# Kernel tuning notes

Measured on AMD Instinct MI355X. Metric: run time of the kernel, lower is better.

The kernel has to match this reference:

```python
import jax, jax.numpy as jnp
import numpy as np

B, N, QD = 2, 1024, 512          # batch (ref+feat), tokens (32x32), query_dim
H, DH = 8, 64                    # heads, dim_head
INNER = H * DH
HW = 64                          # raw mask spatial size
SCALE = DH ** (-0.5)


def setup_inputs() -> dict:
    key = jax.random.key(0)
    ks = jax.random.split(key, 6)
    s = 0.02
    x = jax.random.normal(ks[0], (B, N, QD), jnp.float32)
    mask = jax.random.randint(ks[1], (B // 2, 1, HW, HW), 0, 2).astype(jnp.float32)
    Wq = jax.random.normal(ks[2], (INNER, QD), jnp.float32) * s
    Wk = jax.random.normal(ks[3], (INNER, QD), jnp.float32) * s
    Wv = jax.random.normal(ks[4], (INNER, QD), jnp.float32) * s
    # zero_module only zeroes to_out at init; use random weights for a meaningful baseline
    Wo = jax.random.normal(ks[5], (QD, INNER), jnp.float32) * s
    bo = jnp.zeros((QD,), jnp.float32)
    return {"x": x, "mask": mask, "Wq": Wq, "Wk": Wk, "Wv": Wv, "Wo": Wo, "bo": bo, "share": 1}


def nearest_resize(m, size):
    # PyTorch F.interpolate(mode='nearest'): src = floor(dst * in/out)
    ih = (jnp.arange(size) * m.shape[-2]) // size
    iw = (jnp.arange(size) * m.shape[-1]) // size
    return m[:, :, ih][:, :, :, iw]


def adain(feat, ref, mask):
    # feat, ref: (b, n, d); mask: (b, n, 1) binary
    ref_std = jnp.std(ref, axis=-2, keepdims=True, ddof=1)   # torch std is unbiased
    ref_mean = jnp.mean(ref, axis=-2, keepdims=True)
    cnt = jnp.sum(mask, axis=-2, keepdims=True)              # (b,1,1)
    f_mean = jnp.sum(feat * mask, axis=-2, keepdims=True) / cnt
    f_var = jnp.sum(mask * (feat - f_mean) ** 2, axis=-2, keepdims=True) / (cnt - 1.0)
    f_std = jnp.sqrt(f_var)
    new = (feat - f_mean) / f_std * ref_std + ref_mean
    return new * mask + feat * (1.0 - mask)


def split_heads(t):
    b, n, _ = t.shape
    return t.reshape(b, n, H, DH).transpose(0, 2, 1, 3).reshape(b * H, n, DH)


def reference(x, mask, Wq, Wk, Wv, Wo, bo, share):
    q = x @ Wq.T
    k = x @ Wk.T
    v = x @ Wv.T
    size = int(N ** 0.5)  # 32
    m = nearest_resize(mask, size).reshape(-1, N, 1)  # (B//2, N, 1)
    ref_k, feat_k = k[: B // 2], k[B // 2:]
    ref_v, feat_v = v[: B // 2], v[B // 2:]
    feat_k = adain(feat_k, ref_k, m)
    feat_v = adain(feat_v, ref_v, m)
    k = jnp.concatenate([ref_k, feat_k], axis=0)
    v = jnp.concatenate([ref_v, feat_v], axis=0)
    k = jnp.concatenate([k, jnp.tile(ref_k, (2, 1, 1))], axis=1)  # (B, 2N, INNER)
    v = jnp.concatenate([v, jnp.tile(ref_v, (2, 1, 1))], axis=1)
    qh, kh, vh = split_heads(q), split_heads(k), split_heads(v)
    sim = jnp.einsum('bid,bjd->bij', qh, kh) * SCALE  # (B*H, N, 2N)
    am = jnp.tile(m, (H, 1, N))                       # (B//2*H, N, N)
    am = (1.0 - am) * (-1e9)
    am = jnp.concatenate([jnp.zeros_like(am), am], axis=0)   # (B*H, N, N)
    am = jnp.concatenate([jnp.zeros_like(am), am], axis=-1)  # (B*H, N, 2N)
    attn = jax.nn.softmax(sim + am, axis=-1)
    out = jnp.einsum('bij,bjd->bid', attn, vh)               # (B*H, N, DH)
    out = out.reshape(B, H, N, DH).transpose(0, 2, 1, 3).reshape(B, N, INNER)
    return out @ Wo.T + bo
```

## Files before the change

### kernel.cpp

```cpp
#include <hip/hip_runtime.h>
#include <math.h>

#define NTOK 1024
#define QDIM 512
#define NH 8
#define DHD 64

using s16x8 = __attribute__((ext_vector_type(8))) short;
using f32x4 = __attribute__((ext_vector_type(4))) float;

__device__ __forceinline__ unsigned short f2bf(float x) {
  union { float f; unsigned u; } v; v.f = x;
  unsigned r = (v.u + 0x7fffu + ((v.u >> 16) & 1u)) >> 16;
  return (unsigned short)r;
}
__device__ __forceinline__ float bf2f(unsigned short h) {
  union { unsigned u; float f; } v; v.u = ((unsigned)h) << 16;
  return v.f;
}
__device__ __forceinline__ unsigned cvt_pk_bf16(float lo, float hi) {
  unsigned r;
  asm volatile("v_cvt_pk_bf16_f32 %0, %1, %2" : "=v"(r) : "v"(lo), "v"(hi));
  return r;
}

__global__ __launch_bounds__(256) void cast_kernel(
    const float* __restrict__ x, const float* __restrict__ Wq, const float* __restrict__ Wk,
    const float* __restrict__ Wv, const float* __restrict__ Wo, unsigned short* __restrict__ dst)
{
  const int tid = blockIdx.x * 256 + threadIdx.x;
  const int e = tid * 4;
  const float* src;
  if (e < 1048576) {
    src = x + e;
  } else {
    const int we = e - 1048576;
    const int wi = we >> 18;
    const int off = we & 262143;
    src = (wi == 0 ? Wq : wi == 1 ? Wk : wi == 2 ? Wv : Wo) + off;
  }
  float4 v = *(const float4*)src;
  ushort4 o;
  o.x = f2bf(v.x); o.y = f2bf(v.y); o.z = f2bf(v.z); o.w = f2bf(v.w);
  *(ushort4*)&dst[e] = o;
}

__global__ __launch_bounds__(256) void proj_mfma_kernel(
    const unsigned short* __restrict__ x_b, const unsigned short* __restrict__ w_b,
    unsigned short* __restrict__ q_b, unsigned short* __restrict__ k_b,
    unsigned short* __restrict__ v_b)
{
  const int w = threadIdx.x >> 6;
  const int l = threadIdx.x & 63;
  const int lq = l & 15, lg = l >> 4;
  const int tile = blockIdx.x * 4 + w;
  const int mat = blockIdx.y >> 3;
  const int h = blockIdx.y & 7;
  const unsigned short* W = w_b + (size_t)mat * 262144 + (size_t)(h * 64) * QDIM;
  const int tok0 = tile * 16;

  const unsigned short* xp = &x_b[(size_t)(tok0 + lq) * QDIM + lg * 8];
  const unsigned short* wp = &W[(size_t)lq * QDIM + lg * 8];

  f32x4 acc[4] = {};
  s16x8 aA, bA[4], aB, bB[4];
  aA = *(const s16x8*)&xp[0];
#pragma unroll
  for (int nf = 0; nf < 4; ++nf) bA[nf] = *(const s16x8*)&wp[(size_t)nf * 16 * QDIM];

  for (int kt = 0; kt < 16; kt += 2) {
    aB = *(const s16x8*)&xp[(kt + 1) * 32];
#pragma unroll
    for (int nf = 0; nf < 4; ++nf) bB[nf] = *(const s16x8*)&wp[(size_t)nf * 16 * QDIM + (kt + 1) * 32];
#pragma unroll
    for (int nf = 0; nf < 4; ++nf)
      acc[nf] = __builtin_amdgcn_mfma_f32_16x16x32_bf16(aA, bA[nf], acc[nf], 0, 0, 0);
    if (kt + 2 < 16) {
      aA = *(const s16x8*)&xp[(kt + 2) * 32];
#pragma unroll
      for (int nf = 0; nf < 4; ++nf) bA[nf] = *(const s16x8*)&wp[(size_t)nf * 16 * QDIM + (kt + 2) * 32];
    }
#pragma unroll
    for (int nf = 0; nf < 4; ++nf)
      acc[nf] = __builtin_amdgcn_mfma_f32_16x16x32_bf16(aB, bB[nf], acc[nf], 0, 0, 0);
  }

  const float scale = (mat == 0) ? 0.125f : 1.0f;
  unsigned short* dst = (mat == 0 ? q_b : mat == 1 ? k_b : v_b);
  const int b = tok0 >> 10;
  const int tl0 = tok0 & 1023;
  unsigned short* dp = dst + (size_t)(b * NH + h) * NTOK * DHD;
#pragma unroll
  for (int nf = 0; nf < 4; ++nf)
#pragma unroll
    for (int r = 0; r < 4; ++r)
      dp[(size_t)(tl0 + lg * 4 + r) * DHD + nf * 16 + lq] = f2bf(acc[nf][r] * scale);
}

__global__ __launch_bounds__(256) void adain_stats_kernel(
    const unsigned short* __restrict__ k_b, const unsigned short* __restrict__ v_b,
    const float* __restrict__ mask, float* __restrict__ stats_p, float* __restrict__ stats_cnt)
{
  const int id = blockIdx.x;
  const int arr = id >> 7, h = (id >> 4) & 7, ch = id & 15;
  const unsigned short* base = arr ? v_b : k_b;
  const unsigned short* refp = base + (size_t)h * 65536;
  const unsigned short* fep  = base + (size_t)(8 + h) * 65536;
  const int t = threadIdx.x, dh = t & 63, ig = t >> 6;

  if (arr == 0 && h == 0 && t < 64) {
    const int tok = ch * 64 + t;
    float c = mask[(tok >> 5) * 128 + (tok & 31) * 2];
#pragma unroll
    for (int off = 1; off < 64; off <<= 1) c += __shfl_xor(c, off);
    if (t == 0) stats_cnt[ch] = c;
  }

  float rs = 0.f, rq = 0.f, fs = 0.f, fq = 0.f;
  for (int i = 0; i < 16; ++i) {
    const int tok = ch * 64 + ig * 16 + i;
    const float rv = bf2f(refp[(size_t)tok * DHD + dh]);
    rs += rv; rq += rv * rv;
    const float fv = bf2f(fep[(size_t)tok * DHD + dh]);
    const float mm = mask[(tok >> 5) * 128 + (tok & 31) * 2];
    fs += mm * fv; fq += mm * fv * fv;
  }
  __shared__ float red[4][256];
  red[0][t] = rs; red[1][t] = rq; red[2][t] = fs; red[3][t] = fq;
  __syncthreads();
  if (ig == 0) {
    rs = red[0][dh] + red[0][dh + 64] + red[0][dh + 128] + red[0][dh + 192];
    rq = red[1][dh] + red[1][dh + 64] + red[1][dh + 128] + red[1][dh + 192];
    fs = red[2][dh] + red[2][dh + 64] + red[2][dh + 128] + red[2][dh + 192];
    fq = red[3][dh] + red[3][dh + 64] + red[3][dh + 128] + red[3][dh + 192];
    float* sp = stats_p + (size_t)id * 256;
    sp[dh] = rs; sp[64 + dh] = rq; sp[128 + dh] = fs; sp[192 + dh] = fq;
  }
}

__global__ __launch_bounds__(256) void adain_apply_kernel(
    unsigned short* __restrict__ k_b, unsigned short* __restrict__ v_b,
    const float* __restrict__ mask, const float* __restrict__ stats_p,
    const float* __restrict__ stats_cnt)
{
  const int id = blockIdx.x;
  const int arr = id >> 7, h = (id >> 4) & 7, ch = id & 15;
  unsigned short* fep = (arr ? v_b : k_b) + (size_t)(8 + h) * 65536;
  const int t = threadIdx.x, dh = t & 63, ig = t >> 6;

  __shared__ float sA[64], sB[64];
  if (t < 64) {
    float cnt = 0.f;
#pragma unroll
    for (int c = 0; c < 16; ++c) cnt += stats_cnt[c];
    const float* sp = stats_p + (size_t)((arr << 7) | (h << 4)) * 256;
    float rs = 0.f, rq = 0.f, fs = 0.f, fq = 0.f;
#pragma unroll
    for (int c = 0; c < 16; ++c) {
      rs += sp[c * 256 + t]; rq += sp[c * 256 + 64 + t];
      fs += sp[c * 256 + 128 + t]; fq += sp[c * 256 + 192 + t];
    }
    const float rmean = rs * (1.0f / 1024.0f);
    const float rstd = sqrtf(fmaxf((rq - 1024.0f * rmean * rmean) * (1.0f / 1023.0f), 0.f));
    const float fmean = fs / cnt;
    const float fstd = sqrtf(fmaxf((fq - cnt * fmean * fmean) / (cnt - 1.0f), 0.f));
    const float a = rstd / fstd;
    sA[t] = a; sB[t] = rmean - fmean * a;
  }
  __syncthreads();
  const float a = sA[dh], bb = sB[dh];
  for (int i = 0; i < 16; ++i) {
    const int tok = ch * 64 + ig * 16 + i;
    if (mask[(tok >> 5) * 128 + (tok & 31) * 2] != 0.f) {
      const float fv = bf2f(fep[(size_t)tok * DHD + dh]);
      fep[(size_t)tok * DHD + dh] = f2bf(fv * a + bb);
    }
  }
}

__global__ __launch_bounds__(256) void vtrans_kernel(const unsigned short* __restrict__ v_b,
                                                     unsigned short* __restrict__ v_bT)
{
  const int bh = blockIdx.y;
  const int tc = blockIdx.x;
  __shared__ unsigned short T[64][72];
  const int t = threadIdx.x;
  {
    const int tok = t >> 2, d0 = (t & 3) * 16;
    const unsigned short* src = v_b + ((size_t)bh * NTOK + tc * 64 + tok) * DHD + d0;
    ushort4 a0 = *(const ushort4*)&src[0];
    ushort4 a1 = *(const ushort4*)&src[4];
    ushort4 a2 = *(const ushort4*)&src[8];
    ushort4 a3 = *(const ushort4*)&src[12];
    T[d0 + 0][tok] = a0.x; T[d0 + 1][tok] = a0.y; T[d0 + 2][tok] = a0.z; T[d0 + 3][tok] = a0.w;
    T[d0 + 4][tok] = a1.x; T[d0 + 5][tok] = a1.y; T[d0 + 6][tok] = a1.z; T[d0 + 7][tok] = a1.w;
    T[d0 + 8][tok] = a2.x; T[d0 + 9][tok] = a2.y; T[d0 +10][tok] = a2.z; T[d0 +11][tok] = a2.w;
    T[d0 +12][tok] = a3.x; T[d0 +13][tok] = a3.y; T[d0 +14][tok] = a3.z; T[d0 +15][tok] = a3.w;
  }
  __syncthreads();
  {
    const int dh = t >> 2, t0 = (t & 3) * 16;
    unsigned short* dst = v_bT + ((size_t)bh * DHD + dh) * NTOK + tc * 64 + t0;
    s16x8 r0 = *(const s16x8*)&T[dh][t0];
    s16x8 r1 = *(const s16x8*)&T[dh][t0 + 8];
    *(s16x8*)&dst[0] = r0;
    *(s16x8*)&dst[8] = r1;
  }
}

__global__ __launch_bounds__(64) void attn_part_kernel(
    const unsigned short* __restrict__ q_b, const unsigned short* __restrict__ k_b,
    const unsigned short* __restrict__ v_bT, const float* __restrict__ mask,
    unsigned short* __restrict__ pO, float* __restrict__ pml)
{
  const int id = blockIdx.x;
  const int bh = id >> 8, b = bh >> 3, h = bh & 7;
  const int qt = (id >> 2) & 63, s = id & 3;
  const int q0 = qt * 16;
  const int l = threadIdx.x, lq = l & 15, lg = l >> 4;

  __shared__ unsigned int P_u[16][36];

  const unsigned short* qrow = q_b + ((size_t)bh * NTOK + q0 + lq) * DHD + lg * 8;
  s16x8 qf0 = *(const s16x8*)&qrow[0];
  s16x8 qf1 = *(const s16x8*)&qrow[32];

  const int qtok = q0 + lq;
  const float mneg = (b == 1) ? (1.0f - mask[(qtok >> 5) * 128 + (qtok & 31) * 2]) * (-1e9f) : 0.0f;

  const size_t own = (size_t)bh * 65536, ref = (size_t)h * 65536;
  const int ntile = (b == 0) ? 4 : 8;
  const int kv0 = s * ((b == 0) ? 256 : 512);

  float mrow = -1e30f, lrow = 0.f;
  f32x4 oacc[4] = {};

  for (int tt = 0; tt < ntile; ++tt) {
    const int kvtok = kv0 + tt * 64;
    const int inref = (kvtok >= NTOK) ? 1 : 0;
    const size_t base = inref ? ref : own;
    const int off = inref ? (kvtok - NTOK) : kvtok;
    const unsigned short* kp = k_b + base + (size_t)off * DHD;
    const unsigned short* vp = v_bT + base + off;

    f32x4 sf[4];
#pragma unroll
    for (int mf = 0; mf < 4; ++mf) {
      s16x8 a0 = *(const s16x8*)&kp[(size_t)(mf * 16 + lq) * DHD + lg * 8];
      s16x8 a1 = *(const s16x8*)&kp[(size_t)(mf * 16 + lq) * DHD + 32 + lg * 8];
      f32x4 z = {};
      z = __builtin_amdgcn_mfma_f32_16x16x32_bf16(a0, qf0, z, 0, 0, 0);
      sf[mf] = __builtin_amdgcn_mfma_f32_16x16x32_bf16(a1, qf1, z, 0, 0, 0);
    }

    const float add = inref ? mneg : 0.0f;
    float tm = -1e30f;
#pragma unroll
    for (int mf = 0; mf < 4; ++mf)
#pragma unroll
      for (int r = 0; r < 4; ++r) { sf[mf][r] += add; tm = fmaxf(tm, sf[mf][r]); }
    tm = fmaxf(tm, __shfl_xor(tm, 16));
    tm = fmaxf(tm, __shfl_xor(tm, 32));

    if (!__all(tm <= mrow + 8.0f)) {
      const float mnew = fmaxf(mrow, tm);
      const float alpha = __expf(mrow - mnew);
      mrow = mnew;
      lrow *= alpha;
      float ar[4];
#pragma unroll
      for (int r = 0; r < 4; ++r) ar[r] = __shfl(alpha, lg * 4 + r, 16);
#pragma unroll
      for (int nf = 0; nf < 4; ++nf)
#pragma unroll
        for (int r = 0; r < 4; ++r) oacc[nf][r] *= ar[r];
    }

    float p[4][4];
    float ps = 0.f;
#pragma unroll
    for (int mf = 0; mf < 4; ++mf)
#pragma unroll
      for (int r = 0; r < 4; ++r) { const float e = __expf(sf[mf][r] - mrow); p[mf][r] = e; ps += e; }
    ps += __shfl_xor(ps, 16);
    ps += __shfl_xor(ps, 32);
    lrow += ps;

#pragma unroll
    for (int mf = 0; mf < 4; ++mf) {
      uint2 wv;
      wv.x = cvt_pk_bf16(p[mf][0], p[mf][1]);
      wv.y = cvt_pk_bf16(p[mf][2], p[mf][3]);
      *(uint2*)&P_u[lq][8 * mf + 2 * lg] = wv;
    }

#pragma unroll
    for (int ks = 0; ks < 2; ++ks) {
      s16x8 pa = *(const s16x8*)&P_u[lq][16 * ks + 4 * lg];
#pragma unroll
      for (int nf = 0; nf < 4; ++nf) {
        s16x8 vb = *(const s16x8*)&vp[(size_t)(nf * 16 + lq) * NTOK + ks * 32 + lg * 8];
        oacc[nf] = __builtin_amdgcn_mfma_f32_16x16x32_bf16(pa, vb, oacc[nf], 0, 0, 0);
      }
    }
  }

  const int u = (bh * 64 + qt) * 4 + s;
  unsigned short* pop = pO + (size_t)u * 1024;
#pragma unroll
  for (int nf = 0; nf < 4; ++nf)
#pragma unroll
    for (int r = 0; r < 4; ++r)
      pop[(size_t)(lg * 4 + r) * DHD + nf * 16 + lq] = f2bf(oacc[nf][r]);
  if (l < 16) {
    pml[(size_t)u * 32 + lq] = mrow;
    pml[(size_t)u * 32 + 16 + lq] = lrow;
  }
}

__global__ __launch_bounds__(64) void attn_merge_kernel(
    const unsigned short* __restrict__ pO, const float* __restrict__ pml,
    unsigned short* __restrict__ o_b)
{
  const int id = blockIdx.x;
  const int bh = id >> 6, qt = id & 63;
  const int l = threadIdx.x, r = l & 15, dblk = l >> 4;
  const int d0 = dblk * 16;
  const int base_u = (bh * 64 + qt) * 4;

  float ms[4], ls[4];
  float M = -1e30f;
#pragma unroll
  for (int s = 0; s < 4; ++s) {
    ms[s] = pml[(size_t)(base_u + s) * 32 + r];
    ls[s] = pml[(size_t)(base_u + s) * 32 + 16 + r];
    M = fmaxf(M, ms[s]);
  }
  float Lsum = 0.f;
  float o[16];
#pragma unroll
  for (int j = 0; j < 16; ++j) o[j] = 0.f;
#pragma unroll
  for (int s = 0; s < 4; ++s) {
    const float alpha = __expf(ms[s] - M);
    Lsum += alpha * ls[s];
    const unsigned short* po = pO + (size_t)(base_u + s) * 1024 + (size_t)r * DHD + d0;
    s16x8 a = *(const s16x8*)&po[0];
    s16x8 c = *(const s16x8*)&po[8];
#pragma unroll
    for (int j = 0; j < 8; ++j) {
      o[j] += alpha * bf2f((unsigned short)a[j]);
      o[8 + j] += alpha * bf2f((unsigned short)c[j]);
    }
  }
  const float inv = 1.0f / Lsum;
  unsigned short* dst = o_b + ((size_t)bh * NTOK + qt * 16 + r) * DHD + d0;
  ushort4 w0, w1, w2, w3;
  w0.x = f2bf(o[0] * inv);  w0.y = f2bf(o[1] * inv);  w0.z = f2bf(o[2] * inv);  w0.w = f2bf(o[3] * inv);
  w1.x = f2bf(o[4] * inv);  w1.y = f2bf(o[5] * inv);  w1.z = f2bf(o[6] * inv);  w1.w = f2bf(o[7] * inv);
  w2.x = f2bf(o[8] * inv);  w2.y = f2bf(o[9] * inv);  w2.z = f2bf(o[10] * inv); w2.w = f2bf(o[11] * inv);
  w3.x = f2bf(o[12] * inv); w3.y = f2bf(o[13] * inv); w3.z = f2bf(o[14] * inv); w3.w = f2bf(o[15] * inv);
  *(ushort4*)&dst[0] = w0; *(ushort4*)&dst[4] = w1;
  *(ushort4*)&dst[8] = w2; *(ushort4*)&dst[12] = w3;
}

__global__ __launch_bounds__(256) void outproj_mfma_kernel(
    const unsigned short* __restrict__ o_b, const unsigned short* __restrict__ Wo_b,
    const float* __restrict__ bo, float* __restrict__ out)
{
  const int w = threadIdx.x >> 6, l = threadIdx.x & 63;
  const int lq = l & 15, lg = l >> 4;
  const int tile = blockIdx.x * 4 + w;
  const int c0 = blockIdx.y * 64;
  const int tok = tile * 16 + lq;
  const int b = tok >> 10, tl = tok & 1023;

  const unsigned short* obase = o_b + (size_t)(b * NH) * NTOK * DHD + (size_t)tl * DHD + lg * 8;
  const unsigned short* wp = &Wo_b[(size_t)(c0 + lq) * QDIM + lg * 8];

#define OP_A(KT) (*(const s16x8*)&obase[(size_t)((KT) >> 1) * NTOK * DHD + ((KT) & 1) * 32])

  f32x4 acc[4] = {};
  s16x8 aA, bA[4], aB, bB[4];
  aA = OP_A(0);
#pragma unroll
  for (int nf = 0; nf < 4; ++nf) bA[nf] = *(const s16x8*)&wp[(size_t)nf * 16 * QDIM];

  for (int kt = 0; kt < 16; kt += 2) {
    aB = OP_A(kt + 1);
#pragma unroll
    for (int nf = 0; nf < 4; ++nf) bB[nf] = *(const s16x8*)&wp[(size_t)nf * 16 * QDIM + (kt + 1) * 32];
#pragma unroll
    for (int nf = 0; nf < 4; ++nf)
      acc[nf] = __builtin_amdgcn_mfma_f32_16x16x32_bf16(aA, bA[nf], acc[nf], 0, 0, 0);
    if (kt + 2 < 16) {
      aA = OP_A(kt + 2);
#pragma unroll
      for (int nf = 0; nf < 4; ++nf) bA[nf] = *(const s16x8*)&wp[(size_t)nf * 16 * QDIM + (kt + 2) * 32];
    }
#pragma unroll
    for (int nf = 0; nf < 4; ++nf)
      acc[nf] = __builtin_amdgcn_mfma_f32_16x16x32_bf16(aB, bB[nf], acc[nf], 0, 0, 0);
  }
#undef OP_A

  const int row0 = tile * 16;
#pragma unroll
  for (int nf = 0; nf < 4; ++nf) {
    const float bv = bo[c0 + nf * 16 + lq];
#pragma unroll
    for (int r = 0; r < 4; ++r)
      out[(size_t)(row0 + lg * 4 + r) * QDIM + c0 + nf * 16 + lq] = acc[nf][r] + bv;
  }
}

extern "C" void kernel_launch(void* const* d_in, const int* in_sizes, int n_in,
                              void* d_out, int out_size, void* d_ws, size_t ws_size,
                              hipStream_t stream) {
  const float* x    = (const float*)d_in[0];
  const float* mask = (const float*)d_in[1];
  const float* Wq   = (const float*)d_in[2];
  const float* Wk   = (const float*)d_in[3];
  const float* Wv   = (const float*)d_in[4];
  const float* Wo   = (const float*)d_in[5];
  const float* bo   = (const float*)d_in[6];
  float* out = (float*)d_out;

  char* ws = (char*)d_ws;
  unsigned short* x_b  = (unsigned short*)ws;
  unsigned short* w_b  = (unsigned short*)(ws + 2097152);
  unsigned short* Wo_b = (unsigned short*)(ws + 2097152 + 3 * 524288);
  unsigned short* q_b  = (unsigned short*)(ws + 4194304);
  unsigned short* k_b  = (unsigned short*)(ws + 6291456);
  unsigned short* v_b  = (unsigned short*)(ws + 8388608);
  unsigned short* v_bT = (unsigned short*)(ws + 10485760);
  unsigned short* o_b  = (unsigned short*)(ws + 12582912);
  unsigned short* pO   = (unsigned short*)(ws + 14680064);
  float* pml       = (float*)(ws + 23068672);
  float* stats_p   = (float*)(ws + 23592960);
  float* stats_cnt = (float*)(ws + 23855104);

  cast_kernel<<<2048, 256, 0, stream>>>(x, Wq, Wk, Wv, Wo, x_b);
  proj_mfma_kernel<<<dim3(32, 24), 256, 0, stream>>>(x_b, w_b, q_b, k_b, v_b);
  adain_stats_kernel<<<256, 256, 0, stream>>>(k_b, v_b, mask, stats_p, stats_cnt);
  adain_apply_kernel<<<256, 256, 0, stream>>>(k_b, v_b, mask, stats_p, stats_cnt);
  vtrans_kernel<<<dim3(16, 16), 256, 0, stream>>>(v_b, v_bT);
  attn_part_kernel<<<4096, 64, 0, stream>>>(q_b, k_b, v_bT, mask, pO, pml);
  attn_merge_kernel<<<1024, 64, 0, stream>>>(pO, pml, o_b);
  outproj_mfma_kernel<<<dim3(32, 8), 256, 0, stream>>>(o_b, Wo_b, bo, out);
}
```

Baseline: 177.4 us.

## Process two query tiles per wave to share K/V loads in split attention

Each wave now handles 32 query rows as two 16-row halves. Every K and V^T fragment it loads feeds MFMAs for both halves, which halves the global K/V traffic per query. Waves are packed four per 256-thread block, and the KV range is split eight ways instead of four, so the merge kernel now combines eight partials per row. The partial buffers grew, so pml and the AdaIN stats are moved onto workspace regions that are dead by then, and registers per wave roughly double.

```diff
diff --git a/kernel.cpp b/kernel.cpp
--- a/kernel.cpp
+++ b/kernel.cpp
@@ -208,113 +208,163 @@
   }
 }
 
-__global__ __launch_bounds__(64) void attn_part_kernel(
+__global__ __launch_bounds__(256, 4) void attn_part_kernel(
     const unsigned short* __restrict__ q_b, const unsigned short* __restrict__ k_b,
     const unsigned short* __restrict__ v_bT, const float* __restrict__ mask,
     unsigned short* __restrict__ pO, float* __restrict__ pml)
 {
-  const int id = blockIdx.x;
-  const int bh = id >> 8, b = bh >> 3, h = bh & 7;
-  const int qt = (id >> 2) & 63, s = id & 3;
-  const int q0 = qt * 16;
-  const int l = threadIdx.x, lq = l & 15, lg = l >> 4;
-
-  __shared__ unsigned int P_u[16][36];
-
-  const unsigned short* qrow = q_b + ((size_t)bh * NTOK + q0 + lq) * DHD + lg * 8;
-  s16x8 qf0 = *(const s16x8*)&qrow[0];
-  s16x8 qf1 = *(const s16x8*)&qrow[32];
-
-  const int qtok = q0 + lq;
-  const float mneg = (b == 1) ? (1.0f - mask[(qtok >> 5) * 128 + (qtok & 31) * 2]) * (-1e9f) : 0.0f;
-
-  const size_t own = (size_t)bh * 65536, ref = (size_t)h * 65536;
-  const int ntile = (b == 0) ? 4 : 8;
-  const int kv0 = s * ((b == 0) ? 256 : 512);
-
-  float mrow = -1e30f, lrow = 0.f;
-  f32x4 oacc[4] = {};
+  const int w = threadIdx.x >> 6;
+  const int unit = blockIdx.x * 4 + w;
+  int b, rr;
+  if (unit < 2048) { b = 1; rr = unit; } else { b = 0; rr = unit - 2048; }
+  const int hh = rr >> 8;
+  const int qb = (rr >> 3) & 31;
+  const int s  = rr & 7;
+  const int bh = b * 8 + hh;
+  const int l = threadIdx.x & 63, lq = l & 15, lg = l >> 4;
+
+  __shared__ unsigned int P_u[4][2][16][36];
+
+  const unsigned short* qbase = q_b + ((size_t)bh * NTOK + qb * 32) * DHD;
+  s16x8 qfA0 = *(const s16x8*)&qbase[(size_t)lq * DHD + lg * 8];
+  s16x8 qfA1 = *(const s16x8*)&qbase[(size_t)lq * DHD + 32 + lg * 8];
+  s16x8 qfB0 = *(const s16x8*)&qbase[(size_t)(16 + lq) * DHD + lg * 8];
+  s16x8 qfB1 = *(const s16x8*)&qbase[(size_t)(16 + lq) * DHD + 32 + lg * 8];
+
+  const int ntile = (b == 0) ? 2 : 4;
+  const int kv0 = s * ntile * 64;
+  const int inref = (b == 1 && kv0 >= NTOK) ? 1 : 0;
+  const int off0 = inref ? (kv0 - NTOK) : kv0;
+  const size_t base = (size_t)(inref ? hh : bh) * 65536;
+  const unsigned short* kbase = k_b + base + (size_t)off0 * DHD;
+  const unsigned short* vbase = v_bT + base + off0;
+
+  float mnegA = 0.f, mnegB = 0.f;
+  if (inref) {
+    const int qA = qb * 32 + lq, qB = qA + 16;
+    mnegA = (1.0f - mask[(qA >> 5) * 128 + (qA & 31) * 2]) * (-1e9f);
+    mnegB = (1.0f - mask[(qB >> 5) * 128 + (qB & 31) * 2]) * (-1e9f);
+  }
+
+  float mrowA = -1e30f, lrowA = 0.f;
+  float mrowB = -1e30f, lrowB = 0.f;
+  f32x4 oA[4] = {}, oB[4] = {};
 
   for (int tt = 0; tt < ntile; ++tt) {
-    const int kvtok = kv0 + tt * 64;
-    const int inref = (kvtok >= NTOK) ? 1 : 0;
-    const size_t base = inref ? ref : own;
-    const int off = inref ? (kvtok - NTOK) : kvtok;
-    const unsigned short* kp = k_b + base + (size_t)off * DHD;
-    const unsigned short* vp = v_bT + base + off;
-
-    f32x4 sf[4];
+    const unsigned short* kp = kbase + (size_t)tt * 64 * DHD;
+    const unsigned short* vp = vbase + tt * 64;
+
+    f32x4 sfA[4], sfB[4];
 #pragma unroll
     for (int mf = 0; mf < 4; ++mf) {
       s16x8 a0 = *(const s16x8*)&kp[(size_t)(mf * 16 + lq) * DHD + lg * 8];
       s16x8 a1 = *(const s16x8*)&kp[(size_t)(mf * 16 + lq) * DHD + 32 + lg * 8];
-      f32x4 z = {};
-      z = __builtin_amdgcn_mfma_f32_16x16x32_bf16(a0, qf0, z, 0, 0, 0);
-      sf[mf] = __builtin_amdgcn_mfma_f32_16x16x32_bf16(a1, qf1, z, 0, 0, 0);
-    }
-
-    const float add = inref ? mneg : 0.0f;
-    float tm = -1e30f;
+      f32x4 z0 = {};
+      z0 = __builtin_amdgcn_mfma_f32_16x16x32_bf16(a0, qfA0, z0, 0, 0, 0);
+      sfA[mf] = __builtin_amdgcn_mfma_f32_16x16x32_bf16(a1, qfA1, z0, 0, 0, 0);
+      f32x4 z1 = {};
+      z1 = __builtin_amdgcn_mfma_f32_16x16x32_bf16(a0, qfB0, z1, 0, 0, 0);
+      sfB[mf] = __builtin_amdgcn_mfma_f32_16x16x32_bf16(a1, qfB1, z1, 0, 0, 0);
+    }
+
+    const float addA = inref ? mnegA : 0.0f;
+    const float addB = inref ? mnegB : 0.0f;
+    float tmA = -1e30f, tmB = -1e30f;
 #pragma unroll
     for (int mf = 0; mf < 4; ++mf)
 #pragma unroll
-      for (int r = 0; r < 4; ++r) { sf[mf][r] += add; tm = fmaxf(tm, sf[mf][r]); }
-    tm = fmaxf(tm, __shfl_xor(tm, 16));
-    tm = fmaxf(tm, __shfl_xor(tm, 32));
-
-    if (!__all(tm <= mrow + 8.0f)) {
-      const float mnew = fmaxf(mrow, tm);
-      const float alpha = __expf(mrow - mnew);
-      mrow = mnew;
-      lrow *= alpha;
+      for (int r = 0; r < 4; ++r) {
+        sfA[mf][r] += addA; tmA = fmaxf(tmA, sfA[mf][r]);
+        sfB[mf][r] += addB; tmB = fmaxf(tmB, sfB[mf][r]);
+      }
+    tmA = fmaxf(tmA, __shfl_xor(tmA, 16));
+    tmA = fmaxf(tmA, __shfl_xor(tmA, 32));
+    tmB = fmaxf(tmB, __shfl_xor(tmB, 16));
+    tmB = fmaxf(tmB, __shfl_xor(tmB, 32));
+
+    if (!__all(tmA <= mrowA + 8.0f)) {
+      const float mnew = fmaxf(mrowA, tmA);
+      const float alpha = __expf(mrowA - mnew);
+      mrowA = mnew;
+      lrowA *= alpha;
       float ar[4];
 #pragma unroll
       for (int r = 0; r < 4; ++r) ar[r] = __shfl(alpha, lg * 4 + r, 16);
 #pragma unroll
       for (int nf = 0; nf < 4; ++nf)
 #pragma unroll
-        for (int r = 0; r < 4; ++r) oacc[nf][r] *= ar[r];
-    }
-
-    float p[4][4];
-    float ps = 0.f;
+        for (int r = 0; r < 4; ++r) oA[nf][r] *= ar[r];
+    }
+    if (!__all(tmB <= mrowB + 8.0f)) {
+      const float mnew = fmaxf(mrowB, tmB);
+      const float alpha = __expf(mrowB - mnew);
+      mrowB = mnew;
+      lrowB *= alpha;
+      float ar[4];
+#pragma unroll
+      for (int r = 0; r < 4; ++r) ar[r] = __shfl(alpha, lg * 4 + r, 16);
+#pragma unroll
+      for (int nf = 0; nf < 4; ++nf)
+#pragma unroll
+        for (int r = 0; r < 4; ++r) oB[nf][r] *= ar[r];
+    }
+
+    float pA[4][4], pB[4][4];
+    float psA = 0.f, psB = 0.f;
 #pragma unroll
     for (int mf = 0; mf < 4; ++mf)
 #pragma unroll
-      for (int r = 0; r < 4; ++r) { const float e = __expf(sf[mf][r] - mrow); p[mf][r] = e; ps += e; }
-    ps += __shfl_xor(ps, 16);
-    ps += __shfl_xor(ps, 32);
-    lrow += ps;
+      for (int r = 0; r < 4; ++r) {
+        const float eA = __expf(sfA[mf][r] - mrowA); pA[mf][r] = eA; psA += eA;
+        const float eB = __expf(sfB[mf][r] - mrowB); pB[mf][r] = eB; psB += eB;
+      }
+    psA += __shfl_xor(psA, 16);
+    psA += __shfl_xor(psA, 32);
+    lrowA += psA;
+    psB += __shfl_xor(psB, 16);
+    psB += __shfl_xor(psB, 32);
+    lrowB += psB;
 
 #pragma unroll
     for (int mf = 0; mf < 4; ++mf) {
-      uint2 wv;
-      wv.x = cvt_pk_bf16(p[mf][0], p[mf][1]);
-      wv.y = cvt_pk_bf16(p[mf][2], p[mf][3]);
-      *(uint2*)&P_u[lq][8 * mf + 2 * lg] = wv;
+      uint2 wa;
+      wa.x = cvt_pk_bf16(pA[mf][0], pA[mf][1]);
+      wa.y = cvt_pk_bf16(pA[mf][2], pA[mf][3]);
+      *(uint2*)&P_u[w][0][lq][8 * mf + 2 * lg] = wa;
+      uint2 wb;
+      wb.x = cvt_pk_bf16(pB[mf][0], pB[mf][1]);
+      wb.y = cvt_pk_bf16(pB[mf][2], pB[mf][3]);
+      *(uint2*)&P_u[w][1][lq][8 * mf + 2 * lg] = wb;
     }
 
 #pragma unroll
     for (int ks = 0; ks < 2; ++ks) {
-      s16x8 pa = *(const s16x8*)&P_u[lq][16 * ks + 4 * lg];
+      s16x8 paA = *(const s16x8*)&P_u[w][0][lq][16 * ks + 4 * lg];
+      s16x8 paB = *(const s16x8*)&P_u[w][1][lq][16 * ks + 4 * lg];
 #pragma unroll
       for (int nf = 0; nf < 4; ++nf) {
         s16x8 vb = *(const s16x8*)&vp[(size_t)(nf * 16 + lq) * NTOK + ks * 32 + lg * 8];
-        oacc[nf] = __builtin_amdgcn_mfma_f32_16x16x32_bf16(pa, vb, oacc[nf], 0, 0, 0);
+        oA[nf] = __builtin_amdgcn_mfma_f32_16x16x32_bf16(paA, vb, oA[nf], 0, 0, 0);
+        oB[nf] = __builtin_amdgcn_mfma_f32_16x16x32_bf16(paB, vb, oB[nf], 0, 0, 0);
       }
     }
   }
 
-  const int u = (bh * 64 + qt) * 4 + s;
-  unsigned short* pop = pO + (size_t)u * 1024;
+  const int u = (bh * 32 + qb) * 8 + s;
+  unsigned short* pop = pO + (size_t)u * 2048;
 #pragma unroll
   for (int nf = 0; nf < 4; ++nf)
 #pragma unroll
-    for (int r = 0; r < 4; ++r)
-      pop[(size_t)(lg * 4 + r) * DHD + nf * 16 + lq] = f2bf(oacc[nf][r]);
+    for (int r = 0; r < 4; ++r) {
+      pop[(size_t)(lg * 4 + r) * DHD + nf * 16 + lq] = f2bf(oA[nf][r]);
+      pop[(size_t)(16 + lg * 4 + r) * DHD + nf * 16 + lq] = f2bf(oB[nf][r]);
+    }
   if (l < 16) {
-    pml[(size_t)u * 32 + lq] = mrow;
-    pml[(size_t)u * 32 + 16 + lq] = lrow;
+    pml[(size_t)u * 64 + lq] = mrowA;
+    pml[(size_t)u * 64 + 16 + lq] = lrowA;
+  } else if (l < 32) {
+    pml[(size_t)u * 64 + 32 + lq] = mrowB;
+    pml[(size_t)u * 64 + 48 + lq] = lrowB;
   }
 }
 
@@ -324,16 +374,19 @@
 {
   const int id = blockIdx.x;
   const int bh = id >> 6, qt = id & 63;
+  const int qb = qt >> 1, half = qt & 1;
   const int l = threadIdx.x, r = l & 15, dblk = l >> 4;
   const int d0 = dblk * 16;
-  const int base_u = (bh * 64 + qt) * 4;
-
-  float ms[4], ls[4];
+  const int u0 = (bh * 32 + qb) * 8;
+  const int mo = half * 32;
+  const int row = half * 16 + r;
+
+  float ms[8], ls[8];
   float M = -1e30f;
 #pragma unroll
-  for (int s = 0; s < 4; ++s) {
-    ms[s] = pml[(size_t)(base_u + s) * 32 + r];
-    ls[s] = pml[(size_t)(base_u + s) * 32 + 16 + r];
+  for (int s = 0; s < 8; ++s) {
+    ms[s] = pml[(size_t)(u0 + s) * 64 + mo + r];
+    ls[s] = pml[(size_t)(u0 + s) * 64 + mo + 16 + r];
     M = fmaxf(M, ms[s]);
   }
   float Lsum = 0.f;
@@ -341,10 +394,10 @@
 #pragma unroll
   for (int j = 0; j < 16; ++j) o[j] = 0.f;
 #pragma unroll
-  for (int s = 0; s < 4; ++s) {
+  for (int s = 0; s < 8; ++s) {
     const float alpha = __expf(ms[s] - M);
     Lsum += alpha * ls[s];
-    const unsigned short* po = pO + (size_t)(base_u + s) * 1024 + (size_t)r * DHD + d0;
+    const unsigned short* po = pO + (size_t)(u0 + s) * 2048 + (size_t)row * DHD + d0;
     s16x8 a = *(const s16x8*)&po[0];
     s16x8 c = *(const s16x8*)&po[8];
 #pragma unroll
@@ -436,16 +489,16 @@
   unsigned short* v_bT = (unsigned short*)(ws + 10485760);
   unsigned short* o_b  = (unsigned short*)(ws + 12582912);
   unsigned short* pO   = (unsigned short*)(ws + 14680064);
-  float* pml       = (float*)(ws + 23068672);
-  float* stats_p   = (float*)(ws + 23592960);
-  float* stats_cnt = (float*)(ws + 23855104);
+  float* pml       = (float*)(ws + 2097152);
+  float* stats_p   = (float*)(ws + 0);
+  float* stats_cnt = (float*)(ws + 262144);
 
   cast_kernel<<<2048, 256, 0, stream>>>(x, Wq, Wk, Wv, Wo, x_b);
   proj_mfma_kernel<<<dim3(32, 24), 256, 0, stream>>>(x_b, w_b, q_b, k_b, v_b);
   adain_stats_kernel<<<256, 256, 0, stream>>>(k_b, v_b, mask, stats_p, stats_cnt);
   adain_apply_kernel<<<256, 256, 0, stream>>>(k_b, v_b, mask, stats_p, stats_cnt);
   vtrans_kernel<<<dim3(16, 16), 256, 0, stream>>>(v_b, v_bT);
-  attn_part_kernel<<<4096, 64, 0, stream>>>(q_b, k_b, v_bT, mask, pO, pml);
+  attn_part_kernel<<<1024, 256, 0, stream>>>(q_b, k_b, v_bT, mask, pO, pml);
   attn_merge_kernel<<<1024, 64, 0, stream>>>(pO, pml, o_b);
   outproj_mfma_kernel<<<dim3(32, 8), 256, 0, stream>>>(o_b, Wo_b, bo, out);
 }
```

New measurement: 161.0 us. -9.2%, faster.
